# Performance work log

Measured on AMD Instinct MI355X. Metric: run time of the kernel, lower is better.

## Reference

```python
import jax, jax.numpy as jnp
import numpy as np

KERNEL_SIZE = 11
SIGMA = 1.5
K1 = 0.01
K2 = 0.03
DATA_RANGE = 1.0


def _gaussian_kernel_2d(kernel_size=KERNEL_SIZE, sigma=SIGMA):
    x = jnp.arange(kernel_size, dtype=jnp.float32) - kernel_size // 2
    k1d = jnp.exp(-0.5 * (x / sigma) ** 2)
    k1d = k1d / k1d.sum()
    k2d = k1d[None, :] * k1d[:, None]
    # OIHW layout, single in/out channel
    return k2d[None, None, :, :]


def _gauss_filter(x, kernel):
    pad = KERNEL_SIZE // 2
    return jax.lax.conv_general_dilated(
        x, kernel,
        window_strides=(1, 1),
        padding=[(pad, pad), (pad, pad)],
        dimension_numbers=('NCHW', 'OIHW', 'NCHW'))


def setup_inputs() -> dict:
    key = jax.random.key(0)
    k1, k2 = jax.random.split(key)
    B, C, H, W = 128, 1, 320, 320
    pred = jax.random.uniform(k1, (B, C, H, W), dtype=jnp.float32)
    target = jax.random.uniform(k2, (B, C, H, W), dtype=jnp.float32)
    return {"pred": pred, "target": target}


def reference(pred, target):
    kernel = _gaussian_kernel_2d()
    mu_x = _gauss_filter(pred, kernel)
    mu_y = _gauss_filter(target, kernel)
    mu_x_sq = mu_x * mu_x
    mu_y_sq = mu_y * mu_y
    mu_xy = mu_x * mu_y
    sigma_x_sq = _gauss_filter(pred * pred, kernel) - mu_x_sq
    sigma_y_sq = _gauss_filter(target * target, kernel) - mu_y_sq
    sigma_xy = _gauss_filter(pred * target, kernel) - mu_xy
    dr = jnp.asarray(DATA_RANGE, dtype=pred.dtype)
    c1 = (K1 * dr) ** 2
    c2 = (K2 * dr) ** 2
    numerator = (2 * mu_xy + c1) * (2 * sigma_xy + c2)
    denominator = (mu_x_sq + mu_y_sq + c1) * (sigma_x_sq + sigma_y_sq + c2)
    ssim_map = numerator / denominator
    return 1.0 - ssim_map.mean()
```

## Files before the change

### kernel.cpp

```cpp
#include <hip/hip_runtime.h>


namespace {
constexpr int W = 320, H = 320, B = 128;
constexpr int TH = 10;
constexpr int NSTRIPE = H / TH;
constexpr int WPB = 4;
constexpr int NWAVE = B * NSTRIPE;
constexpr int NBLK = NWAVE / WPB;
constexpr int ITERS = TH / 2;
constexpr float C1 = 1.0e-4f;
constexpr float C2 = 9.0e-4f;
constexpr int NSLOT = 128;
constexpr int SSTR = 16;
}

typedef _Float16 h2 __attribute__((ext_vector_type(2)));

__device__ __forceinline__ float fdot2f(h2 a, h2 b, float c) {
#if __has_builtin(__builtin_amdgcn_fdot2)
  return __builtin_amdgcn_fdot2(a, b, c, false);
#else
  return fmaf((float)a.x, (float)b.x, fmaf((float)a.y, (float)b.y, c));
#endif
}

__device__ __forceinline__ float rcpf(float x) {
  float r;
  asm("v_rcp_f32 %0, %1" : "=v"(r) : "v"(x));
  return r;
}

__device__ __forceinline__ h2 pack2(float a, float b) {
  return h2{(_Float16)a, (_Float16)b};
}

__device__ __forceinline__ h2 pkrtz(float a, float b) {
#if __has_builtin(__builtin_amdgcn_cvt_pkrtz)
  return __builtin_bit_cast(h2, __builtin_amdgcn_cvt_pkrtz(a, b));
#else
  return pack2(a, b);
#endif
}

__device__ __forceinline__ h2 dpp_up1(h2 v) {
  int r = __builtin_amdgcn_update_dpp(0, __builtin_bit_cast(int, v),
                                      0x138, 0xF, 0xF, true);
  return __builtin_bit_cast(h2, r);
}
__device__ __forceinline__ h2 dpp_dn1(h2 v) {
  int r = __builtin_amdgcn_update_dpp(0, __builtin_bit_cast(int, v),
                                      0x130, 0xF, 0xF, true);
  return __builtin_bit_cast(h2, r);
}

#define LOADP_RAW(ROW, A0, B0, A1, B1)                                        \
  do {                                                                        \
    const int r0_ = (ROW);                                                    \
    if (r0_ >= 0 && r0_ < H) {                                                \
      const float* p_ = P + r0_ * W;                                          \
      const float* t_ = T + r0_ * W;                                          \
      _Pragma("unroll") for (int c_ = 0; c_ < 5; ++c_) {                      \
        A0[c_] = p_[c_]; B0[c_] = t_[c_];                                     \
      }                                                                       \
    } else {                                                                  \
      _Pragma("unroll") for (int c_ = 0; c_ < 5; ++c_) {                      \
        A0[c_] = 0.f; B0[c_] = 0.f;                                           \
      }                                                                       \
    }                                                                         \
    if (r0_ + 1 >= 0 && r0_ + 1 < H) {                                        \
      const float* p_ = P + (r0_ + 1) * W;                                    \
      const float* t_ = T + (r0_ + 1) * W;                                    \
      _Pragma("unroll") for (int c_ = 0; c_ < 5; ++c_) {                      \
        A1[c_] = p_[c_]; B1[c_] = t_[c_];                                     \
      }                                                                       \
    } else {                                                                  \
      _Pragma("unroll") for (int c_ = 0; c_ < 5; ++c_) {                      \
        A1[c_] = 0.f; B1[c_] = 0.f;                                           \
      }                                                                       \
    }                                                                         \
  } while (0)

#define PACKTO(J, A0, B0, A1, B1)                                             \
  do {                                                                        \
    _Pragma("unroll") for (int c_ = 0; c_ < 5; ++c_) {                        \
      rp[J][c_] = pkrtz(A0[c_], A1[c_]);                                      \
      rt[J][c_] = pkrtz(B0[c_], B1[c_]);                                      \
    }                                                                         \
  } while (0)

#define HALO(PKc, L, R)                                                       \
  do {                                                                        \
    _Pragma("unroll") for (int c_ = 0; c_ < 5; ++c_) {                        \
      L[c_] = dpp_up1(PKc[c_]);                                               \
      R[c_] = dpp_dn1(PKc[c_]);                                               \
    }                                                                         \
  } while (0)

#define HBLUR(PKc, L, R, O)                                                   \
  do {                                                                        \
    _Pragma("unroll") for (int c_ = 0; c_ < 5; ++c_) {                        \
      h2 s1_ = WH[0] * ((c_ + 0 < 5) ? L[c_] : PKc[c_ - 5]);                  \
      _Pragma("unroll") for (int k_ = 1; k_ < 5; ++k_) {                      \
        const int i_ = c_ + k_;                                               \
        s1_ = WH[k_] * ((i_ < 5) ? L[i_] : PKc[i_ - 5]) + s1_;                \
      }                                                                       \
      h2 s2_ = WH[10] * R[c_];                                                \
      _Pragma("unroll") for (int k_ = 9; k_ >= 5; --k_) {                     \
        const int i_ = c_ + k_;                                               \
        s2_ = WH[k_] * ((i_ < 10) ? PKc[i_ - 5] : R[i_ - 10]) + s2_;          \
      }                                                                       \
      O[c_] = s1_ + s2_;                                                      \
    }                                                                         \
  } while (0)

__global__ __launch_bounds__(256) void ssim_main(
    const float* __restrict__ pred, const float* __restrict__ targ,
    float* __restrict__ sink, int slotmask, int sstr) {
  const int lane = threadIdx.x & 63;
  const int wid  = threadIdx.x >> 6;
  const int stripe = blockIdx.x * WPB + wid;
  const int img = stripe / NSTRIPE;
  const int y0  = (stripe % NSTRIPE) * TH;

  const float* __restrict__ P = pred + (size_t)img * (W * H) + 5 * lane;
  const float* __restrict__ T = targ + (size_t)img * (W * H) + 5 * lane;

  constexpr float WF[11] = {0.00102838f, 0.00759885f, 0.03600081f, 0.10936069f,
                            0.21300553f, 0.26601171f, 0.21300553f, 0.10936069f,
                            0.03600081f, 0.00759885f, 0.00102838f};
  const h2 wAv[6] = {pack2(WF[0], WF[1]),  pack2(WF[2], WF[3]),
                     pack2(WF[4], WF[5]),  pack2(WF[6], WF[7]),
                     pack2(WF[8], WF[9]),  pack2(WF[10], 0.f)};
  const h2 wBv[6] = {pack2(0.f, WF[0]),    pack2(WF[1], WF[2]),
                     pack2(WF[3], WF[4]),  pack2(WF[5], WF[6]),
                     pack2(WF[7], WF[8]),  pack2(WF[9], WF[10])};
  h2 WH[11];
#pragma unroll
  for (int k = 0; k < 11; ++k) WH[k] = pack2(WF[k], WF[k]);

  h2 rp[6][5], rt[6][5];
  float nfA[5], ntA[5], nfB[5], ntB[5];

  {
    float aA[5], bA[5], cA[5], dA[5];
    float aB[5], bB[5], cB[5], dB[5];
    LOADP_RAW(y0 - 5, aA, bA, cA, dA);
    LOADP_RAW(y0 - 3, aB, bB, cB, dB);
    PACKTO(1, aA, bA, cA, dA);
    LOADP_RAW(y0 - 1, aA, bA, cA, dA);
    PACKTO(2, aB, bB, cB, dB);
    LOADP_RAW(y0 + 1, aB, bB, cB, dB);
    PACKTO(3, aA, bA, cA, dA);
    LOADP_RAW(y0 + 3, aA, bA, cA, dA);
    PACKTO(4, aB, bB, cB, dB);
    LOADP_RAW(y0 + 5, nfA, ntA, nfB, ntB);
    PACKTO(5, aA, bA, cA, dA);
  }

  float acc = 0.f;

#pragma unroll 1
  for (int it = 0; it < ITERS; ++it) {
#pragma unroll
    for (int j = 0; j < 5; ++j)
#pragma unroll
      for (int c = 0; c < 5; ++c) {
        rp[j][c] = rp[j + 1][c];
        rt[j][c] = rt[j + 1][c];
      }
    PACKTO(5, nfA, ntA, nfB, ntB);
    if (it + 1 < ITERS) LOADP_RAW(y0 + 2 * it + 7, nfA, ntA, nfB, ntB);

    h2 PK[5][5];
#pragma unroll
    for (int c = 0; c < 5; ++c) {
      float mpA = 0, mtA = 0, ppA = 0, ttA = 0, ptA = 0;
      float mpB = 0, mtB = 0, ppB = 0, ttB = 0, ptB = 0;
#pragma unroll
      for (int j = 0; j < 6; ++j) {
        const h2 a = rp[j][c], b = rt[j][c];
        const h2 aa = a * a, bb = b * b, ab = a * b;
        const h2 wa = wAv[j], wb = wBv[j];
        mpA = fdot2f(wa, a, mpA);
        mtA = fdot2f(wa, b, mtA);
        ppA = fdot2f(wa, aa, ppA);
        ttA = fdot2f(wa, bb, ttA);
        ptA = fdot2f(wa, ab, ptA);
        mpB = fdot2f(wb, a, mpB);
        mtB = fdot2f(wb, b, mtB);
        ppB = fdot2f(wb, aa, ppB);
        ttB = fdot2f(wb, bb, ttB);
        ptB = fdot2f(wb, ab, ptB);
      }
      PK[0][c] = pkrtz(mpA, mpB);
      PK[1][c] = pkrtz(mtA, mtB);
      PK[2][c] = pkrtz(ppA, ppB);
      PK[3][c] = pkrtz(ttA, ttB);
      PK[4][c] = pkrtz(ptA, ptB);
    }

    h2 OUT[5][5];
#pragma unroll
    for (int ch = 0; ch < 5; ++ch) {
      h2 L[5], R[5];
      HALO(PK[ch], L, R);
      HBLUR(PK[ch], L, R, OUT[ch]);
    }

#pragma unroll
    for (int c = 0; c < 5; ++c) {
#pragma unroll
      for (int r = 0; r < 2; ++r) {
        const float mx = r ? (float)OUT[0][c].y : (float)OUT[0][c].x;
        const float my = r ? (float)OUT[1][c].y : (float)OUT[1][c].x;
        const float xx = r ? (float)OUT[2][c].y : (float)OUT[2][c].x;
        const float yy = r ? (float)OUT[3][c].y : (float)OUT[3][c].x;
        const float xy = r ? (float)OUT[4][c].y : (float)OUT[4][c].x;
        const float mxx = mx * mx, myy = my * my, mxy = mx * my;
        const float vx = xx - mxx, vy = yy - myy, vxy = xy - mxy;
        const float num = (2.f * mxy + C1) * (2.f * vxy + C2);
        const float den = (mxx + myy + C1) * (vx + vy + C2);
        acc = fmaf(num, rcpf(den), acc);
      }
    }
  }

#pragma unroll
  for (int off = 32; off; off >>= 1) acc += __shfl_xor(acc, off, 64);
  if (lane == 0) atomicAdd(sink + (stripe & slotmask) * sstr, acc);
}

__global__ void ssim_final(const float* __restrict__ sink, int nslot, int sstr,
                           float* __restrict__ out) {
  const int tid = threadIdx.x;
  float v = 0.f;
  for (int s = tid; s < nslot; s += 64) v += sink[s * sstr];
#pragma unroll
  for (int off = 32; off; off >>= 1) v += __shfl_xor(v, off, 64);
  if (tid == 0) out[0] = 1.f - v / 13107200.f;
}

extern "C" void kernel_launch(void* const* d_in, const int* in_sizes, int n_in,
                              void* d_out, int out_size, void* d_ws, size_t ws_size,
                              hipStream_t stream) {
  (void)in_sizes; (void)n_in; (void)out_size;
  const float* pred = (const float*)d_in[0];
  const float* targ = (const float*)d_in[1];
  float* out = (float*)d_out;

  float* sink;
  int nslot, sstr;
  const size_t need = (size_t)NSLOT * SSTR * sizeof(float);
  if (ws_size >= need) {
    sink = (float*)d_ws;
    nslot = NSLOT;
    sstr = SSTR;
  } else {
    sink = out;
    nslot = 1;
    sstr = 0;
  }
  (void)hipMemsetAsync(sink, 0, nslot == 1 ? sizeof(float) : need, stream);
  ssim_main<<<dim3(NBLK), dim3(256), 0, stream>>>(pred, targ, sink, nslot - 1, sstr);
  ssim_final<<<1, 64, 0, stream>>>(sink, nslot, sstr, out);
}
```

Baseline: 60.85 us.

## Shrink row stripes to four rows with fully unrolled two-step compute

```diff
diff --git a/kernel.cpp b/kernel.cpp
--- a/kernel.cpp
+++ b/kernel.cpp
@@ -3,12 +3,11 @@
 
 namespace {
 constexpr int W = 320, H = 320, B = 128;
-constexpr int TH = 10;
+constexpr int TH = 4;
 constexpr int NSTRIPE = H / TH;
 constexpr int WPB = 4;
 constexpr int NWAVE = B * NSTRIPE;
 constexpr int NBLK = NWAVE / WPB;
-constexpr int ITERS = TH / 2;
 constexpr float C1 = 1.0e-4f;
 constexpr float C2 = 9.0e-4f;
 constexpr int NSLOT = 128;
@@ -43,6 +42,11 @@
 #endif
 }
 
+__device__ __forceinline__ h2 sgh2(h2 v) {
+  return __builtin_bit_cast(
+      h2, __builtin_amdgcn_readfirstlane(__builtin_bit_cast(int, v)));
+}
+
 __device__ __forceinline__ h2 dpp_up1(h2 v) {
   int r = __builtin_amdgcn_update_dpp(0, __builtin_bit_cast(int, v),
                                       0x138, 0xF, 0xF, true);
@@ -114,7 +118,56 @@
     }                                                                         \
   } while (0)
 
-__global__ __launch_bounds__(256) void ssim_main(
+#define COMPUTE(I)                                                            \
+  do {                                                                        \
+    h2 PK[5][5];                                                              \
+    _Pragma("unroll") for (int c = 0; c < 5; ++c) {                           \
+      float mpA = 0, mtA = 0, ppA = 0, ttA = 0, ptA = 0;                      \
+      float mpB = 0, mtB = 0, ppB = 0, ttB = 0, ptB = 0;                      \
+      _Pragma("unroll") for (int j = 0; j < 6; ++j) {                         \
+        const h2 a = rp[(I) + j][c], b = rt[(I) + j][c];                      \
+        const h2 aa = a * a, bb = b * b, ab = a * b;                          \
+        const h2 wa = wAv[j], wb = wBv[j];                                    \
+        mpA = fdot2f(wa, a, mpA);                                             \
+        mtA = fdot2f(wa, b, mtA);                                             \
+        ppA = fdot2f(wa, aa, ppA);                                            \
+        ttA = fdot2f(wa, bb, ttA);                                            \
+        ptA = fdot2f(wa, ab, ptA);                                            \
+        mpB = fdot2f(wb, a, mpB);                                             \
+        mtB = fdot2f(wb, b, mtB);                                             \
+        ppB = fdot2f(wb, aa, ppB);                                            \
+        ttB = fdot2f(wb, bb, ttB);                                            \
+        ptB = fdot2f(wb, ab, ptB);                                            \
+      }                                                                       \
+      PK[0][c] = pkrtz(mpA, mpB);                                             \
+      PK[1][c] = pkrtz(mtA, mtB);                                             \
+      PK[2][c] = pkrtz(ppA, ppB);                                             \
+      PK[3][c] = pkrtz(ttA, ttB);                                             \
+      PK[4][c] = pkrtz(ptA, ptB);                                             \
+    }                                                                         \
+    h2 OUT[5][5];                                                             \
+    _Pragma("unroll") for (int ch = 0; ch < 5; ++ch) {                        \
+      h2 L[5], R[5];                                                          \
+      HALO(PK[ch], L, R);                                                     \
+      HBLUR(PK[ch], L, R, OUT[ch]);                                           \
+    }                                                                         \
+    _Pragma("unroll") for (int c = 0; c < 5; ++c) {                           \
+      _Pragma("unroll") for (int r = 0; r < 2; ++r) {                         \
+        const float mx = r ? (float)OUT[0][c].y : (float)OUT[0][c].x;         \
+        const float my = r ? (float)OUT[1][c].y : (float)OUT[1][c].x;         \
+        const float xx = r ? (float)OUT[2][c].y : (float)OUT[2][c].x;         \
+        const float yy = r ? (float)OUT[3][c].y : (float)OUT[3][c].x;         \
+        const float xy = r ? (float)OUT[4][c].y : (float)OUT[4][c].x;         \
+        const float mxx = mx * mx, myy = my * my, mxy = mx * my;              \
+        const float vx = xx - mxx, vy = yy - myy, vxy = xy - mxy;             \
+        const float num = fmaf(2.f, mxy, C1) * fmaf(2.f, vxy, C2);            \
+        const float den = (mxx + myy + C1) * (vx + vy + C2);                  \
+        acc = fmaf(num, rcpf(den), acc);                                      \
+      }                                                                       \
+    }                                                                         \
+  } while (0)
+
+__global__ __launch_bounds__(256, 4) void ssim_main(
     const float* __restrict__ pred, const float* __restrict__ targ,
     float* __restrict__ sink, int slotmask, int sstr) {
   const int lane = threadIdx.x & 63;
@@ -129,102 +182,40 @@
   constexpr float WF[11] = {0.00102838f, 0.00759885f, 0.03600081f, 0.10936069f,
                             0.21300553f, 0.26601171f, 0.21300553f, 0.10936069f,
                             0.03600081f, 0.00759885f, 0.00102838f};
-  const h2 wAv[6] = {pack2(WF[0], WF[1]),  pack2(WF[2], WF[3]),
-                     pack2(WF[4], WF[5]),  pack2(WF[6], WF[7]),
-                     pack2(WF[8], WF[9]),  pack2(WF[10], 0.f)};
-  const h2 wBv[6] = {pack2(0.f, WF[0]),    pack2(WF[1], WF[2]),
-                     pack2(WF[3], WF[4]),  pack2(WF[5], WF[6]),
-                     pack2(WF[7], WF[8]),  pack2(WF[9], WF[10])};
+  const h2 wAv[6] = {sgh2(pack2(WF[0], WF[1])),  sgh2(pack2(WF[2], WF[3])),
+                     sgh2(pack2(WF[4], WF[5])),  sgh2(pack2(WF[6], WF[7])),
+                     sgh2(pack2(WF[8], WF[9])),  sgh2(pack2(WF[10], 0.f))};
+  const h2 wBv[6] = {sgh2(pack2(0.f, WF[0])),    sgh2(pack2(WF[1], WF[2])),
+                     sgh2(pack2(WF[3], WF[4])),  sgh2(pack2(WF[5], WF[6])),
+                     sgh2(pack2(WF[7], WF[8])),  sgh2(pack2(WF[9], WF[10]))};
   h2 WH[11];
 #pragma unroll
-  for (int k = 0; k < 11; ++k) WH[k] = pack2(WF[k], WF[k]);
-
-  h2 rp[6][5], rt[6][5];
-  float nfA[5], ntA[5], nfB[5], ntB[5];
+  for (int k = 0; k < 11; ++k) WH[k] = sgh2(pack2(WF[k], WF[k]));
+
+  h2 rp[7][5], rt[7][5];
 
   {
     float aA[5], bA[5], cA[5], dA[5];
     float aB[5], bB[5], cB[5], dB[5];
     LOADP_RAW(y0 - 5, aA, bA, cA, dA);
     LOADP_RAW(y0 - 3, aB, bB, cB, dB);
-    PACKTO(1, aA, bA, cA, dA);
+    PACKTO(0, aA, bA, cA, dA);
     LOADP_RAW(y0 - 1, aA, bA, cA, dA);
-    PACKTO(2, aB, bB, cB, dB);
+    PACKTO(1, aB, bB, cB, dB);
     LOADP_RAW(y0 + 1, aB, bB, cB, dB);
-    PACKTO(3, aA, bA, cA, dA);
+    PACKTO(2, aA, bA, cA, dA);
     LOADP_RAW(y0 + 3, aA, bA, cA, dA);
-    PACKTO(4, aB, bB, cB, dB);
-    LOADP_RAW(y0 + 5, nfA, ntA, nfB, ntB);
-    PACKTO(5, aA, bA, cA, dA);
+    PACKTO(3, aB, bB, cB, dB);
+    LOADP_RAW(y0 + 5, aB, bB, cB, dB);
+    PACKTO(4, aA, bA, cA, dA);
+    LOADP_RAW(y0 + 7, aA, bA, cA, dA);
+    PACKTO(5, aB, bB, cB, dB);
+    PACKTO(6, aA, bA, cA, dA);
   }
 
   float acc = 0.f;
-
-#pragma unroll 1
-  for (int it = 0; it < ITERS; ++it) {
-#pragma unroll
-    for (int j = 0; j < 5; ++j)
-#pragma unroll
-      for (int c = 0; c < 5; ++c) {
-        rp[j][c] = rp[j + 1][c];
-        rt[j][c] = rt[j + 1][c];
-      }
-    PACKTO(5, nfA, ntA, nfB, ntB);
-    if (it + 1 < ITERS) LOADP_RAW(y0 + 2 * it + 7, nfA, ntA, nfB, ntB);
-
-    h2 PK[5][5];
-#pragma unroll
-    for (int c = 0; c < 5; ++c) {
-      float mpA = 0, mtA = 0, ppA = 0, ttA = 0, ptA = 0;
-      float mpB = 0, mtB = 0, ppB = 0, ttB = 0, ptB = 0;
-#pragma unroll
-      for (int j = 0; j < 6; ++j) {
-        const h2 a = rp[j][c], b = rt[j][c];
-        const h2 aa = a * a, bb = b * b, ab = a * b;
-        const h2 wa = wAv[j], wb = wBv[j];
-        mpA = fdot2f(wa, a, mpA);
-        mtA = fdot2f(wa, b, mtA);
-        ppA = fdot2f(wa, aa, ppA);
-        ttA = fdot2f(wa, bb, ttA);
-        ptA = fdot2f(wa, ab, ptA);
-        mpB = fdot2f(wb, a, mpB);
-        mtB = fdot2f(wb, b, mtB);
-        ppB = fdot2f(wb, aa, ppB);
-        ttB = fdot2f(wb, bb, ttB);
-        ptB = fdot2f(wb, ab, ptB);
-      }
-      PK[0][c] = pkrtz(mpA, mpB);
-      PK[1][c] = pkrtz(mtA, mtB);
-      PK[2][c] = pkrtz(ppA, ppB);
-      PK[3][c] = pkrtz(ttA, ttB);
-      PK[4][c] = pkrtz(ptA, ptB);
-    }
-
-    h2 OUT[5][5];
-#pragma unroll
-    for (int ch = 0; ch < 5; ++ch) {
-      h2 L[5], R[5];
-      HALO(PK[ch], L, R);
-      HBLUR(PK[ch], L, R, OUT[ch]);
-    }
-
-#pragma unroll
-    for (int c = 0; c < 5; ++c) {
-#pragma unroll
-      for (int r = 0; r < 2; ++r) {
-        const float mx = r ? (float)OUT[0][c].y : (float)OUT[0][c].x;
-        const float my = r ? (float)OUT[1][c].y : (float)OUT[1][c].x;
-        const float xx = r ? (float)OUT[2][c].y : (float)OUT[2][c].x;
-        const float yy = r ? (float)OUT[3][c].y : (float)OUT[3][c].x;
-        const float xy = r ? (float)OUT[4][c].y : (float)OUT[4][c].x;
-        const float mxx = mx * mx, myy = my * my, mxy = mx * my;
-        const float vx = xx - mxx, vy = yy - myy, vxy = xy - mxy;
-        const float num = (2.f * mxy + C1) * (2.f * vxy + C2);
-        const float den = (mxx + myy + C1) * (vx + vy + C2);
-        acc = fmaf(num, rcpf(den), acc);
-      }
-    }
-  }
+  COMPUTE(0);
+  COMPUTE(1);
 
 #pragma unroll
   for (int off = 32; off; off >>= 1) acc += __shfl_xor(acc, off, 64);
@@ -235,7 +226,7 @@
                            float* __restrict__ out) {
   const int tid = threadIdx.x;
   float v = 0.f;
-  for (int s = tid; s < nslot; s += 64) v += sink[s * sstr];
+  for (int q = tid; q < nslot; q += 64) v += sink[q * sstr];
 #pragma unroll
   for (int off = 32; off; off >>= 1) v += __shfl_xor(v, off, 64);
   if (tid == 0) out[0] = 1.f - v / 13107200.f;
```

Measured after the change: 86.15 us. 41.6% more time.
